# Optimization experiments

Measured on AMD Instinct MI355X. Metric: run time of the kernel, lower is better.

The kernel has to match this reference:

```python
import jax, jax.numpy as jnp
import numpy as np

GROUPS = 8   # GroupNorm groups used by create_pat_conv*_blocks(..., groups=8)
EPS = 1e-5
K = 20       # num_neighbor


def group_norm(x, gamma, beta):
    # x: [B, C, ...spatial]
    B, C = x.shape[0], x.shape[1]
    shape = x.shape
    xg = x.reshape(B, GROUPS, C // GROUPS, -1)
    m = xg.mean(axis=(2, 3), keepdims=True)
    v = ((xg - m) ** 2).mean(axis=(2, 3), keepdims=True)
    xg = (xg - m) * jax.lax.rsqrt(v + EPS)
    x = xg.reshape(shape)
    bshape = (1, C) + (1,) * (len(shape) - 2)
    return x * gamma.reshape(bshape) + beta.reshape(bshape)


def conv_block(x, w, b, gamma, beta):
    # pointwise (kernel-size 1) conv + GroupNorm + ELU, works for 1d and 2d spatial
    y = jnp.einsum('oc,bc...->bo...', w, x) + b.reshape((1, -1) + (1,) * (x.ndim - 2))
    return jax.nn.elu(group_norm(y, gamma, beta))


def knn_graph(points, k):
    # points: [B, 3, N] -> neighbor coords [B, 3, N, k] (self included, dilation=1)
    sq = jnp.sum(points * points, axis=1)                      # [B, N]
    inner = jnp.einsum('bci,bcj->bij', points, points)         # [B, N, N]
    dist = sq[:, :, None] + sq[:, None, :] - 2.0 * inner       # squared pairwise dist
    _, idx = jax.lax.top_k(-dist, k)                           # [B, N, k] smallest dists
    neighbors = jnp.take_along_axis(points[:, :, None, :], idx[:, None, :, :], axis=3)
    return neighbors                                           # [B, 3, N, k]


def setup_inputs() -> dict:
    key = jax.random.key(0)
    B, N = 4, 8192
    dims1 = [6, 32, 64]
    dims2 = [64, 512, 1024]
    keys = iter(jax.random.split(key, 32))
    inp = {"points": jax.random.normal(next(keys), (B, 3, N), dtype=jnp.float32)}
    for tag, dims in (("p1", dims1), ("p2", dims2)):
        for i in range(len(dims) - 1):
            cin, cout = dims[i], dims[i + 1]
            inp[f"{tag}_w{i}"] = jax.random.normal(next(keys), (cout, cin), dtype=jnp.float32) / np.float32(np.sqrt(cin))
            inp[f"{tag}_b{i}"] = jnp.zeros((cout,), dtype=jnp.float32)
            inp[f"{tag}_g{i}"] = jnp.ones((cout,), dtype=jnp.float32)
            inp[f"{tag}_beta{i}"] = jnp.zeros((cout,), dtype=jnp.float32)
    return inp


def reference(points, p1_w0, p1_b0, p1_g0, p1_beta0, p1_w1, p1_b1, p1_g1, p1_beta1,
              p2_w0, p2_b0, p2_g0, p2_beta0, p2_w1, p2_b1, p2_g1, p2_beta1):
    neighbors = knn_graph(points, K)                             # [B, 3, N, K]
    center = jnp.broadcast_to(points[:, :, :, None], neighbors.shape)
    x = jnp.concatenate([center, neighbors - center], axis=1)   # [B, 6, N, K]
    x = conv_block(x, p1_w0, p1_b0, p1_g0, p1_beta0)            # [B, 32, N, K]
    x = conv_block(x, p1_w1, p1_b1, p1_g1, p1_beta1)            # [B, 64, N, K]
    x = jnp.max(x, axis=2)                                      # [B, 64, K] (faithful to source: max over dim=2)
    x = conv_block(x, p2_w0, p2_b0, p2_g0, p2_beta0)            # [B, 512, K]
    x = conv_block(x, p2_w1, p2_b1, p2_g1, p2_beta1)            # [B, 1024, K]
    return x
```

## Files before the change

kernel.cpp:

```cpp
#include <hip/hip_runtime.h>
#include <math.h>

#define NPTS   8192
#define BATCH  4
#define KNN    20
#define NKTOT  (NPTS*KNN)
#define EPS    1e-5f
#define QC     28

typedef float v2f __attribute__((ext_vector_type(2)));

__device__ __forceinline__ float elu(float x) { return x > 0.0f ? x : expm1f(x); }
__device__ __forceinline__ float eluf(float x) { return x > 0.0f ? x : __expf(x) - 1.0f; }
__device__ __forceinline__ v2f splat2(float x) { v2f v; v.x = x; v.y = x; return v; }
__device__ __forceinline__ float rfl(float x) {
    return __uint_as_float(__builtin_amdgcn_readfirstlane(__float_as_uint(x)));
}

__device__ __forceinline__ unsigned fenc(float f) {
    unsigned b = __float_as_uint(f);
    return b ^ ((unsigned)(((int)b) >> 31) | 0x80000000u);
}
__device__ __forceinline__ float fdec(unsigned u) {
    unsigned b = (u & 0x80000000u) ? (u ^ 0x80000000u) : ~u;
    return __uint_as_float(b);
}

__global__ __launch_bounds__(256) void prep_kernel(const float* __restrict__ points,
                                                   float4* __restrict__ pts4)
{
    const int t = blockIdx.x * 256 + threadIdx.x;
    const int b = t >> 13, n = t & (NPTS - 1);
    const float* px = points + b * 3 * NPTS;
    float x = px[n], y = px[NPTS + n], z = px[2 * NPTS + n];
    pts4[t] = make_float4(x, y, z, -0.5f * (x * x + y * y + z * z));
}

__global__ __launch_bounds__(256, 8) void knn_kernel(const float4* __restrict__ pts4,
                                                     int* __restrict__ idx_out)
{
    __shared__ unsigned long long queue[32][QC];
    __shared__ float smaxs[4][8][64];
    __shared__ float gates[2][8];
    __shared__ int qcnt[32];

    const int tid  = threadIdx.x;
    const int lane = tid & 63;
    const int wv   = tid >> 6;
    const int oct  = wv >> 1;
    const int par  = wv & 1;
    const int b    = blockIdx.x >> 9;
    const int q0   = (blockIdx.x & 511) * 16 + oct * 8;
    const float4* pb = pts4 + b * NPTS;
    const int cbase = par * (NPTS / 2);

    if (tid < 32) qcnt[tid] = 0;

    float qx[8], qy[8], qz[8];
    v2f smax2[8];
#pragma unroll
    for (int q = 0; q < 8; ++q) {
        float4 qp = pb[q0 + q];
        qx[q] = rfl(qp.x); qy[q] = rfl(qp.y); qz[q] = rfl(qp.z);
        smax2[q] = splat2(-INFINITY);
    }

#pragma unroll 4
    for (int t = 0; t < NPTS / 2 / 128; ++t) {
        float4 p0 = pb[cbase + t * 128 + 2 * lane];
        float4 p1 = pb[cbase + t * 128 + 2 * lane + 1];
        v2f px = { p0.x, p1.x }, py = { p0.y, p1.y };
        v2f pz = { p0.z, p1.z }, pw = { p0.w, p1.w };
#pragma unroll
        for (int q = 0; q < 8; ++q) {
            v2f sv = __builtin_elementwise_fma(splat2(qx[q]), px,
                     __builtin_elementwise_fma(splat2(qy[q]), py,
                     __builtin_elementwise_fma(splat2(qz[q]), pz, pw)));
            smax2[q] = __builtin_elementwise_max(smax2[q], sv);
        }
    }
#pragma unroll
    for (int q = 0; q < 8; ++q) smaxs[wv][q][lane] = fmaxf(smax2[q].x, smax2[q].y);
    __syncthreads();

#pragma unroll
    for (int qq = 0; qq < 4; ++qq) {
        const int q = par * 4 + qq;
        float v = fmaxf(smaxs[2 * oct][q][lane], smaxs[2 * oct + 1][q][lane]);
#pragma unroll
        for (int k = 2; k <= 64; k <<= 1)
#pragma unroll
            for (int j = k >> 1; j >= 1; j >>= 1) {
                float o = __shfl_xor(v, j);
                bool up = ((lane & k) == 0);
                bool keepmin = (((lane & j) == 0) == up);
                v = keepmin ? fminf(v, o) : fmaxf(v, o);
            }
        float m = __shfl(v, 44);
        if (lane == 0) gates[oct][q] = m - 1e-4f - 1e-5f * fabsf(m);
    }
    __syncthreads();
    float sgate[8];
#pragma unroll
    for (int q = 0; q < 8; ++q) sgate[q] = gates[oct][q];

    for (int t = 0; t < NPTS / 2 / 128; ++t) {
        float4 p0 = pb[cbase + t * 128 + 2 * lane];
        float4 p1 = pb[cbase + t * 128 + 2 * lane + 1];
        v2f px = { p0.x, p1.x }, py = { p0.y, p1.y };
        v2f pz = { p0.z, p1.z }, pw = { p0.w, p1.w };
        const int jb = cbase + t * 128 + 2 * lane;
#pragma unroll
        for (int q = 0; q < 8; ++q) {
            v2f sv = __builtin_elementwise_fma(splat2(qx[q]), px,
                     __builtin_elementwise_fma(splat2(qy[q]), py,
                     __builtin_elementwise_fma(splat2(qz[q]), pz, pw)));
            if (fmaxf(sv.x, sv.y) >= sgate[q]) {
#pragma unroll
                for (int h = 0; h < 2; ++h) {
                    float svh = h ? sv.y : sv.x;
                    if (svh >= sgate[q]) {
                        int slot = atomicAdd(&qcnt[wv * 8 + q], 1);
                        if (slot < QC) {
                            unsigned long long key =
                                ((unsigned long long)fenc(svh) << 32)
                                | (unsigned)(NPTS - 1 - (jb + h));
                            queue[wv * 8 + q][slot] = key;
                        }
                    }
                }
            }
        }
    }
    __syncthreads();

#pragma unroll
    for (int qq = 0; qq < 4; ++qq) {
        const int q = par * 4 + qq;
        int cA = qcnt[(2 * oct) * 8 + q];     cA = cA < QC ? cA : QC;
        int cB = qcnt[(2 * oct + 1) * 8 + q]; cB = cB < QC ? cB : QC;
        unsigned long long key = 0ull;
        if (lane < cA)           key = queue[(2 * oct) * 8 + q][lane];
        else if (lane < cA + cB) key = queue[(2 * oct + 1) * 8 + q][lane - cA];
#pragma unroll
        for (int k = 2; k <= 64; k <<= 1)
#pragma unroll
            for (int j = k >> 1; j >= 1; j >>= 1) {
                unsigned long long o = __shfl_xor(key, j);
                bool up = ((lane & k) == 0);
                bool keepmax = (((lane & j) == 0) == up);
                bool omax = o > key;
                key = (keepmax == omax) ? o : key;
            }
        if (lane < KNN)
            idx_out[(b * KNN + lane) * NPTS + (q0 + q)] =
                NPTS - 1 - (int)(unsigned)(key & 0xFFFFFFFFu);
    }
}

__global__ __launch_bounds__(256) void moments_x_kernel(const float4* __restrict__ pts4,
                                                        const int* __restrict__ idx,
                                                        float* __restrict__ sums1p)
{
    const int b  = blockIdx.x / 80;
    const int r0 = (blockIdx.x - b * 80) * 2048;
    const float4* pb = pts4 + b * NPTS;
    const int* ib = idx + b * NKTOT;

    float v[27];
#pragma unroll
    for (int i = 0; i < 27; ++i) v[i] = 0.f;

    for (int e = 0; e < 8; ++e) {
        const int id = r0 + e * 256 + threadIdx.x;
        const int n = id & (NPTS - 1);
        const int j = ib[id];
        float4 c4 = pb[n];
        float4 e4 = pb[j];
        float x[6] = { c4.x, c4.y, c4.z, e4.x - c4.x, e4.y - c4.y, e4.z - c4.z };
        int p = 6;
#pragma unroll
        for (int d = 0; d < 6; ++d) {
            v[d] += x[d];
#pragma unroll
            for (int ee = d; ee < 6; ++ee) v[p++] += x[d] * x[ee];
        }
    }
#pragma unroll
    for (int i = 0; i < 27; ++i)
        for (int o = 32; o > 0; o >>= 1) v[i] += __shfl_xor(v[i], o);

    __shared__ float red[4][27];
    const int lane = threadIdx.x & 63, w = threadIdx.x >> 6;
    if (lane == 0)
#pragma unroll
        for (int i = 0; i < 27; ++i) red[w][i] = v[i];
    __syncthreads();
    if (threadIdx.x < 27) {
        float acc = red[0][threadIdx.x] + red[1][threadIdx.x] + red[2][threadIdx.x] + red[3][threadIdx.x];
        int slot = blockIdx.x & 63;
        atomicAdd(&sums1p[(slot * BATCH + b) * 27 + threadIdx.x], acc);
    }
}

__global__ void finalize1_kernel(const float* __restrict__ sums1p,
                                 const float* __restrict__ w1, const float* __restrict__ b1,
                                 const float* __restrict__ g1, const float* __restrict__ beta1,
                                 float* __restrict__ w1f)
{
    __shared__ float S[BATCH][27];
    const int t = threadIdx.x;
    if (t < 108) {
        int b = t / 27, i = t % 27;
        float acc = 0.f;
        for (int s = 0; s < 64; ++s) acc += sums1p[(s * BATCH + b) * 27 + i];
        S[b][i] = acc;
    }
    __syncthreads();
    const int b = t >> 5, c = t & 31;
    const float invS = 1.0f / (float)NKTOT;
    float Ex[6], M[6][6];
#pragma unroll
    for (int d = 0; d < 6; ++d) Ex[d] = S[b][d] * invS;
    int p = 6;
#pragma unroll
    for (int d = 0; d < 6; ++d)
#pragma unroll
        for (int e = d; e < 6; ++e) { float v = S[b][p++] * invS; M[d][e] = v; M[e][d] = v; }
    const int g = c >> 2;
    float msum = 0.f, qsum = 0.f;
    for (int cc = g * 4; cc < g * 4 + 4; ++cc) {
        float w[6];
#pragma unroll
        for (int d = 0; d < 6; ++d) w[d] = w1[cc * 6 + d];
        float dotEx = 0.f;
#pragma unroll
        for (int d = 0; d < 6; ++d) dotEx += w[d] * Ex[d];
        float Ey = dotEx + b1[cc];
        float Ey2 = 0.f;
#pragma unroll
        for (int d = 0; d < 6; ++d)
#pragma unroll
            for (int e = 0; e < 6; ++e) Ey2 += w[d] * w[e] * M[d][e];
        Ey2 += 2.0f * b1[cc] * dotEx + b1[cc] * b1[cc];
        msum += Ey; qsum += Ey2;
    }
    float m = msum * 0.25f;
    float var = qsum * 0.25f - m * m;
    float inv = rsqrtf(var + EPS);
    float s = g1[c] * inv;
    float tt = s * (b1[c] - m) + beta1[c];
    float* o = w1f + (b * 32 + c) * 8;
#pragma unroll
    for (int d = 0; d < 6; ++d) o[d] = s * w1[c * 6 + d];
    o[6] = tt; o[7] = 0.f;
}

__global__ __launch_bounds__(256, 5) void fused_main_kernel(
    const float4* __restrict__ pts4, const int* __restrict__ idxb,
    const float* __restrict__ w1f, const float* __restrict__ w2, const float* __restrict__ b2,
    float* __restrict__ sums2p, unsigned int* __restrict__ maxenc, unsigned int* __restrict__ minenc)
{
    __shared__ __align__(16) float w2t[32 * 64];
    __shared__ __align__(16) float z1s[32 * 128];
    __shared__ __align__(16) float4 w1s4[64];
    __shared__ float b2s[64];
    __shared__ float redmx[256], redmn[256], sqred[128];

    const int t   = threadIdx.x;
    const int blk = blockIdx.x;
    const int nc  = blk & 15;
    const int k   = (blk >> 4) % 20;
    const int b   = blk / 320;

    for (int i = t; i < 512; i += 256) {
        float4 v = ((const float4*)w2)[i];
        int c = i >> 3, kq = (i & 7) * 4;
        w2t[(kq + 0) * 64 + c] = v.x; w2t[(kq + 1) * 64 + c] = v.y;
        w2t[(kq + 2) * 64 + c] = v.z; w2t[(kq + 3) * 64 + c] = v.w;
    }
    if (t < 64) { w1s4[t] = ((const float4*)w1f)[b * 64 + t]; b2s[t] = b2[t]; }

    const int wvi  = t >> 6;
    const int nf   = t & 127;
    const int cgf  = t >> 7;
    const int cq   = t & 15;
    const int ng   = t >> 4;
    const int c0   = cq * 4;
    const int n0   = ng * 8;
    const float4* pb = pts4 + b * NPTS;
    const int nbase = nc * 512;
    const int* idxrow = idxb + (b * KNN + k) * NPTS;

    float mx[4], mn[4];
#pragma unroll
    for (int ci = 0; ci < 4; ++ci) { mx[ci] = -INFINITY; mn[ci] = INFINITY; }
    float gs = 0.f, gq = 0.f;

    for (int ph = 0; ph < 4; ++ph) {
        const int n = nbase + ph * 128 + nf;
        const int j = idxrow[n];
        float4 c4 = pb[n];
        float4 e4 = pb[j];
        float x0[6] = { c4.x, c4.y, c4.z, e4.x - c4.x, e4.y - c4.y, e4.z - c4.z };

        __syncthreads();
#pragma unroll
        for (int jj = 0; jj < 16; ++jj) {
            int c = cgf * 16 + jj;
            float4 wA = w1s4[c * 2 + 0];
            float4 wB = w1s4[c * 2 + 1];
            float z = wB.z;
            z = fmaf(wA.x, x0[0], z); z = fmaf(wA.y, x0[1], z); z = fmaf(wA.z, x0[2], z);
            z = fmaf(wA.w, x0[3], z); z = fmaf(wB.x, x0[4], z); z = fmaf(wB.y, x0[5], z);
            z1s[c * 128 + nf] = eluf(z);
        }
        __syncthreads();

        float acc[4][8];
#pragma unroll
        for (int ci = 0; ci < 4; ++ci) {
            float bb = b2s[c0 + ci];
#pragma unroll
            for (int pj = 0; pj < 8; ++pj) acc[ci][pj] = bb;
        }
#pragma unroll
        for (int kk = 0; kk < 32; ++kk) {
            float4 av = *(const float4*)&w2t[kk * 64 + c0];
            float4 z0 = *(const float4*)&z1s[kk * 128 + n0];
            float4 z1v = *(const float4*)&z1s[kk * 128 + n0 + 4];
            float avv[4] = { av.x, av.y, av.z, av.w };
            float zvv[8] = { z0.x, z0.y, z0.z, z0.w, z1v.x, z1v.y, z1v.z, z1v.w };
#pragma unroll
            for (int ci = 0; ci < 4; ++ci)
#pragma unroll
                for (int pj = 0; pj < 8; ++pj) acc[ci][pj] = fmaf(avv[ci], zvv[pj], acc[ci][pj]);
        }
#pragma unroll
        for (int ci = 0; ci < 4; ++ci)
#pragma unroll
            for (int pj = 0; pj < 8; ++pj) {
                float v = acc[ci][pj];
                gs += v; gq = fmaf(v, v, gq);
                mx[ci] = fmaxf(mx[ci], v); mn[ci] = fminf(mn[ci], v);
            }
    }

#pragma unroll
    for (int m = 16; m <= 32; m <<= 1) {
#pragma unroll
        for (int ci = 0; ci < 4; ++ci) {
            mx[ci] = fmaxf(mx[ci], __shfl_xor(mx[ci], m));
            mn[ci] = fminf(mn[ci], __shfl_xor(mn[ci], m));
        }
        gs += __shfl_xor(gs, m);
        gq += __shfl_xor(gq, m);
    }
    if ((t & 63) < 16) {
#pragma unroll
        for (int ci = 0; ci < 4; ++ci) {
            redmx[wvi * 64 + cq * 4 + ci] = mx[ci];
            redmn[wvi * 64 + cq * 4 + ci] = mn[ci];
        }
        sqred[(wvi * 16 + cq) * 2 + 0] = gs;
        sqred[(wvi * 16 + cq) * 2 + 1] = gq;
    }
    __syncthreads();
    if (t < 64) {
        float m = fmaxf(fmaxf(redmx[t], redmx[64 + t]), fmaxf(redmx[128 + t], redmx[192 + t]));
        atomicMax(&maxenc[(b * 64 + t) * KNN + k], fenc(m));
    } else if (t < 128) {
        int c = t - 64;
        float m = fminf(fminf(redmn[c], redmn[64 + c]), fminf(redmn[128 + c], redmn[192 + c]));
        atomicMin(&minenc[(b * 64 + c) * KNN + k], fenc(m));
    } else if (t < 144) {
        int i2 = t - 128, g = i2 >> 1, w = i2 & 1;
        float v = 0.f;
#pragma unroll
        for (int wv2 = 0; wv2 < 4; ++wv2)
            v += sqred[(wv2 * 16 + 2 * g) * 2 + w] + sqred[(wv2 * 16 + 2 * g + 1) * 2 + w];
        int slot = blk & 63;
        atomicAdd(&sums2p[((slot * BATCH + b) * 8 + g) * 2 + w], v);
    }
}

__global__ void build_m1_kernel(const float* __restrict__ sums2p,
                                const unsigned int* __restrict__ maxenc,
                                const unsigned int* __restrict__ minenc,
                                const float* __restrict__ gamma, const float* __restrict__ beta,
                                float* __restrict__ m1)
{
    const int t = blockIdx.x * 256 + threadIdx.x;
    const int b = t / 1280;
    const int r = t - b * 1280;
    const int c = r / 20;
    const int g = c >> 3;
    float s = 0.f, q = 0.f;
    for (int sl = 0; sl < 64; ++sl) {
        s += sums2p[((sl * BATCH + b) * 8 + g) * 2 + 0];
        q += sums2p[((sl * BATCH + b) * 8 + g) * 2 + 1];
    }
    const float cnt = 8.0f * (float)NKTOT;
    float m = s / cnt;
    float var = q / cnt - m * m;
    float inv = rsqrtf(var + EPS);
    float sc = gamma[c] * inv;
    float tt = beta[c] - sc * m;
    float y = (sc >= 0.f) ? fdec(maxenc[t]) : fdec(minenc[t]);
    m1[t] = elu(sc * y + tt);
}

template <int CIN, int SLOTS>
__global__ void p2_gemm_kernel(const float* __restrict__ zin, const float* __restrict__ w,
                               const float* __restrict__ bias, float* __restrict__ yout,
                               float* __restrict__ sumsp, int chans_per_group)
{
    const int t = blockIdx.x * 256 + threadIdx.x;
    const int per_b = (gridDim.x * 256) / BATCH;
    const int b = t / per_b;
    const int r = t - b * per_b;
    const int o = r / 20;
    const int k = r - o * 20;
    const float* zb = zin + b * CIN * 20;
    const float* wrow = w + o * CIN;
    float acc = bias[o];
    for (int c = 0; c < CIN; c += 4) {
        float4 wv = *(const float4*)&wrow[c];
        acc += wv.x * zb[(c + 0) * 20 + k] + wv.y * zb[(c + 1) * 20 + k]
             + wv.z * zb[(c + 2) * 20 + k] + wv.w * zb[(c + 3) * 20 + k];
    }
    yout[t] = acc;

    __shared__ float ls[16];
    if (threadIdx.x < 16) ls[threadIdx.x] = 0.f;
    __syncthreads();
    const int g = o / chans_per_group;
    atomicAdd(&ls[g * 2 + 0], acc);
    atomicAdd(&ls[g * 2 + 1], acc * acc);
    __syncthreads();
    if (threadIdx.x < 16) {
        int slot = blockIdx.x & (SLOTS - 1);
        atomicAdd(&sumsp[(slot * BATCH + b) * 16 + threadIdx.x], ls[threadIdx.x]);
    }
}

template <int SLOTS>
__global__ void p2_finalize_kernel(const float* __restrict__ y, const float* __restrict__ sumsp,
                                   const float* __restrict__ gamma, const float* __restrict__ beta,
                                   float* __restrict__ z, int chans_per_group, float cnt)
{
    const int t = blockIdx.x * 256 + threadIdx.x;
    const int per_b = (gridDim.x * 256) / BATCH;
    const int b = t / per_b;
    const int r = t - b * per_b;
    const int o = r / 20;
    const int g = o / chans_per_group;
    float s = 0.f, q = 0.f;
    for (int sl = 0; sl < SLOTS; ++sl) {
        s += sumsp[(sl * BATCH + b) * 16 + g * 2 + 0];
        q += sumsp[(sl * BATCH + b) * 16 + g * 2 + 1];
    }
    float m = s / cnt;
    float var = q / cnt - m * m;
    float inv = rsqrtf(var + EPS);
    float v = gamma[o] * inv * (y[t] - m) + beta[o];
    z[t] = elu(v);
}

extern "C" void kernel_launch(void* const* d_in, const int* in_sizes, int n_in,
                              void* d_out, int out_size, void* d_ws, size_t ws_size,
                              hipStream_t stream)
{
    const float* points  = (const float*)d_in[0];
    const float* p1_w0   = (const float*)d_in[1];
    const float* p1_b0   = (const float*)d_in[2];
    const float* p1_g0   = (const float*)d_in[3];
    const float* p1_bt0  = (const float*)d_in[4];
    const float* p1_w1   = (const float*)d_in[5];
    const float* p1_b1   = (const float*)d_in[6];
    const float* p1_g1   = (const float*)d_in[7];
    const float* p1_bt1  = (const float*)d_in[8];
    const float* p2_w0   = (const float*)d_in[9];
    const float* p2_b0   = (const float*)d_in[10];
    const float* p2_g0   = (const float*)d_in[11];
    const float* p2_bt0  = (const float*)d_in[12];
    const float* p2_w1   = (const float*)d_in[13];
    const float* p2_b1   = (const float*)d_in[14];
    const float* p2_g1   = (const float*)d_in[15];
    const float* p2_bt1  = (const float*)d_in[16];
    float* out = (float*)d_out;

    float* ws = (float*)d_ws;
    int*      idx     = (int*)ws;
    float*    sums1p  = ws + 655360;
    float*    sums2p  = sums1p + 6912;
    float*    sumsAp  = sums2p + 4096;
    float*    sumsBp  = sumsAp + 1024;
    unsigned* maxenc  = (unsigned*)(sumsBp + 1024);
    unsigned* minenc  = maxenc + 5120;
    float*    w1f     = (float*)(minenc + 5120);
    float*    m1      = w1f + 1024;
    float*    yp2a    = m1 + 5120;
    float*    zp2a    = yp2a + 40960;
    float*    yp2b    = zp2a + 40960;
    float4*   pts4    = (float4*)yp2a;

    hipMemsetAsync(sums1p, 0, (6912 + 4096 + 1024 + 1024 + 5120) * sizeof(float), stream);
    hipMemsetAsync(minenc, 0xFF, 5120 * sizeof(unsigned), stream);

    prep_kernel<<<128, 256, 0, stream>>>(points, pts4);
    knn_kernel<<<2048, 256, 0, stream>>>(pts4, idx);
    moments_x_kernel<<<320, 256, 0, stream>>>(pts4, idx, sums1p);
    finalize1_kernel<<<1, 128, 0, stream>>>(sums1p, p1_w0, p1_b0, p1_g0, p1_bt0, w1f);
    fused_main_kernel<<<1280, 256, 0, stream>>>(pts4, idx, w1f, p1_w1, p1_b1,
                                                sums2p, maxenc, minenc);
    build_m1_kernel<<<20, 256, 0, stream>>>(sums2p, maxenc, minenc, p1_g1, p1_bt1, m1);
    p2_gemm_kernel<64, 16><<<160, 256, 0, stream>>>(m1, p2_w0, p2_b0, yp2a, sumsAp, 64);
    p2_finalize_kernel<16><<<160, 256, 0, stream>>>(yp2a, sumsAp, p2_g0, p2_bt0, zp2a, 64, 1280.0f);
    p2_gemm_kernel<512, 16><<<320, 256, 0, stream>>>(zp2a, p2_w1, p2_b1, yp2b, sumsBp, 128);
    p2_finalize_kernel<16><<<320, 256, 0, stream>>>(yp2b, sumsBp, p2_g1, p2_bt1, out, 128, 2560.0f);
}
```

Before: 264.3 us.

## Split KNN candidate scan across four waves per query octet and prefetch gathers

Each KNN block now handles 8 queries instead of 16, and all four waves scan a quarter of the candidates for the same 8 queries. The launch grid doubles to 4096 blocks and the per-wave candidate queue shrinks from 28 to 16 slots, merged across four queues before the bitonic sort. This shortens each wave's serial scan and raises parallelism, at the cost of reloading query points in more blocks and a higher chance of overflowing the smaller queue. Separately, the fused main kernel loads all neighbor indices up front and prefetches the next phase's center and neighbor points during compute, to hide gather latency.

```diff
diff --git a/kernel.cpp b/kernel.cpp
--- a/kernel.cpp
+++ b/kernel.cpp
@@ -6,7 +6,7 @@
 #define KNN    20
 #define NKTOT  (NPTS*KNN)
 #define EPS    1e-5f
-#define QC     28
+#define QC2    16
 
 typedef float v2f __attribute__((ext_vector_type(2)));
 
@@ -39,20 +39,18 @@
 __global__ __launch_bounds__(256, 8) void knn_kernel(const float4* __restrict__ pts4,
                                                      int* __restrict__ idx_out)
 {
-    __shared__ unsigned long long queue[32][QC];
+    __shared__ unsigned long long queue[32][QC2];
     __shared__ float smaxs[4][8][64];
-    __shared__ float gates[2][8];
+    __shared__ float gates[8];
     __shared__ int qcnt[32];
 
     const int tid  = threadIdx.x;
     const int lane = tid & 63;
     const int wv   = tid >> 6;
-    const int oct  = wv >> 1;
-    const int par  = wv & 1;
-    const int b    = blockIdx.x >> 9;
-    const int q0   = (blockIdx.x & 511) * 16 + oct * 8;
+    const int b    = blockIdx.x >> 10;
+    const int q0   = (blockIdx.x & 1023) * 8;
     const float4* pb = pts4 + b * NPTS;
-    const int cbase = par * (NPTS / 2);
+    const int cbase = wv * (NPTS / 4);
 
     if (tid < 32) qcnt[tid] = 0;
 
@@ -66,7 +64,7 @@
     }
 
 #pragma unroll 4
-    for (int t = 0; t < NPTS / 2 / 128; ++t) {
+    for (int t = 0; t < NPTS / 4 / 128; ++t) {
         float4 p0 = pb[cbase + t * 128 + 2 * lane];
         float4 p1 = pb[cbase + t * 128 + 2 * lane + 1];
         v2f px = { p0.x, p1.x }, py = { p0.y, p1.y };
@@ -84,9 +82,10 @@
     __syncthreads();
 
 #pragma unroll
-    for (int qq = 0; qq < 4; ++qq) {
-        const int q = par * 4 + qq;
-        float v = fmaxf(smaxs[2 * oct][q][lane], smaxs[2 * oct + 1][q][lane]);
+    for (int qq = 0; qq < 2; ++qq) {
+        const int q = wv * 2 + qq;
+        float v = fmaxf(fmaxf(smaxs[0][q][lane], smaxs[1][q][lane]),
+                        fmaxf(smaxs[2][q][lane], smaxs[3][q][lane]));
 #pragma unroll
         for (int k = 2; k <= 64; k <<= 1)
 #pragma unroll
@@ -97,14 +96,14 @@
                 v = keepmin ? fminf(v, o) : fmaxf(v, o);
             }
         float m = __shfl(v, 44);
-        if (lane == 0) gates[oct][q] = m - 1e-4f - 1e-5f * fabsf(m);
+        if (lane == 0) gates[q] = m - 1e-4f - 1e-5f * fabsf(m);
     }
     __syncthreads();
     float sgate[8];
 #pragma unroll
-    for (int q = 0; q < 8; ++q) sgate[q] = gates[oct][q];
-
-    for (int t = 0; t < NPTS / 2 / 128; ++t) {
+    for (int q = 0; q < 8; ++q) sgate[q] = gates[q];
+
+    for (int t = 0; t < NPTS / 4 / 128; ++t) {
         float4 p0 = pb[cbase + t * 128 + 2 * lane];
         float4 p1 = pb[cbase + t * 128 + 2 * lane + 1];
         v2f px = { p0.x, p1.x }, py = { p0.y, p1.y };
@@ -121,7 +120,7 @@
                     float svh = h ? sv.y : sv.x;
                     if (svh >= sgate[q]) {
                         int slot = atomicAdd(&qcnt[wv * 8 + q], 1);
-                        if (slot < QC) {
+                        if (slot < QC2) {
                             unsigned long long key =
                                 ((unsigned long long)fenc(svh) << 32)
                                 | (unsigned)(NPTS - 1 - (jb + h));
@@ -135,13 +134,18 @@
     __syncthreads();
 
 #pragma unroll
-    for (int qq = 0; qq < 4; ++qq) {
-        const int q = par * 4 + qq;
-        int cA = qcnt[(2 * oct) * 8 + q];     cA = cA < QC ? cA : QC;
-        int cB = qcnt[(2 * oct + 1) * 8 + q]; cB = cB < QC ? cB : QC;
+    for (int qq = 0; qq < 2; ++qq) {
+        const int q = wv * 2 + qq;
+        int c0 = qcnt[0 * 8 + q];  c0 = c0 < QC2 ? c0 : QC2;
+        int c1 = qcnt[1 * 8 + q];  c1 = c1 < QC2 ? c1 : QC2;
+        int c2 = qcnt[2 * 8 + q];  c2 = c2 < QC2 ? c2 : QC2;
+        int c3 = qcnt[3 * 8 + q];  c3 = c3 < QC2 ? c3 : QC2;
+        int b1 = c0, b2 = c0 + c1, b3 = c0 + c1 + c2, b4 = b3 + c3;
         unsigned long long key = 0ull;
-        if (lane < cA)           key = queue[(2 * oct) * 8 + q][lane];
-        else if (lane < cA + cB) key = queue[(2 * oct + 1) * 8 + q][lane - cA];
+        if (lane < b1)      key = queue[0 * 8 + q][lane];
+        else if (lane < b2) key = queue[1 * 8 + q][lane - b1];
+        else if (lane < b3) key = queue[2 * 8 + q][lane - b2];
+        else if (lane < b4) key = queue[3 * 8 + q][lane - b3];
 #pragma unroll
         for (int k = 2; k <= 64; k <<= 1)
 #pragma unroll
@@ -292,16 +296,18 @@
     const int nbase = nc * 512;
     const int* idxrow = idxb + (b * KNN + k) * NPTS;
 
+    int jv[4];
+#pragma unroll
+    for (int ph = 0; ph < 4; ++ph) jv[ph] = idxrow[nbase + ph * 128 + nf];
+    float4 c4 = pb[nbase + nf];
+    float4 e4 = pb[jv[0]];
+
     float mx[4], mn[4];
 #pragma unroll
     for (int ci = 0; ci < 4; ++ci) { mx[ci] = -INFINITY; mn[ci] = INFINITY; }
     float gs = 0.f, gq = 0.f;
 
     for (int ph = 0; ph < 4; ++ph) {
-        const int n = nbase + ph * 128 + nf;
-        const int j = idxrow[n];
-        float4 c4 = pb[n];
-        float4 e4 = pb[j];
         float x0[6] = { c4.x, c4.y, c4.z, e4.x - c4.x, e4.y - c4.y, e4.z - c4.z };
 
         __syncthreads();
@@ -316,6 +322,11 @@
             z1s[c * 128 + nf] = eluf(z);
         }
         __syncthreads();
+
+        if (ph < 3) {
+            c4 = pb[nbase + (ph + 1) * 128 + nf];
+            e4 = pb[jv[ph + 1]];
+        }
 
         float acc[4][8];
 #pragma unroll
@@ -509,7 +520,7 @@
     hipMemsetAsync(minenc, 0xFF, 5120 * sizeof(unsigned), stream);
 
     prep_kernel<<<128, 256, 0, stream>>>(points, pts4);
-    knn_kernel<<<2048, 256, 0, stream>>>(pts4, idx);
+    knn_kernel<<<4096, 256, 0, stream>>>(pts4, idx);
     moments_x_kernel<<<320, 256, 0, stream>>>(pts4, idx, sums1p);
     finalize1_kernel<<<1, 128, 0, stream>>>(sums1p, p1_w0, p1_b0, p1_g0, p1_bt0, w1f);
     fused_main_kernel<<<1280, 256, 0, stream>>>(pts4, idx, w1f, p1_w1, p1_b1,
```

New measurement: 266.5 us. Within noise of the previous version (+0.9%).
